# Performance work log

Hardware: AMD Instinct MI355X
Metric: run time of the kernel (lower is better)

## Reference

```python
import jax, jax.numpy as jnp
import numpy as np

N, H, DH = 8, 12, 64          # batch, heads, head dim (embedding_dim=768)
LV, LA = 1568, 512            # video / audio token counts
NCV, NCA = 392, 256           # candidates kept: LV*(1-0.75), LA*(1-0.5)
SCALE = DH ** -0.5            # avmatching_module.scale


def setup_inputs() -> dict:
    key = jax.random.key(0)
    ks = jax.random.split(key, 14)
    f32 = jnp.float32
    return {
        "pos_v_q": jax.random.normal(ks[0], (N, H, LV, DH), f32),
        "pos_v_k": jax.random.normal(ks[1], (N, H, LV, DH), f32),
        "pos_a_q": jax.random.normal(ks[2], (N, H, LA, DH), f32),
        "pos_a_k": jax.random.normal(ks[3], (N, H, LA, DH), f32),
        "pos_cross_att_av": jax.random.uniform(ks[4], (N, H, LA, LV), f32),
        "pos_cross_att_va": jax.random.uniform(ks[5], (N, H, LV, LA), f32),
        "n_attn_av": jax.random.uniform(ks[6], (N, LV), f32, 0.01, 1.0),
        "n_attn_va": jax.random.uniform(ks[7], (N, LA), f32, 0.01, 1.0),
        "spu_a_cls": jax.random.normal(ks[8], (N, H, DH), f32),
        "spu_v_cls": jax.random.normal(ks[9], (N, H, DH), f32),
        "u_v": jax.random.uniform(ks[10], (N, LV), f32),
        "u_a": jax.random.uniform(ks[11], (N, LA), f32),
        # att ids come from argsort of attention scores in the original -> permutations
        "att_av_ids": jnp.argsort(jax.random.uniform(ks[12], (N, LV)), axis=1),
        "att_va_ids": jnp.argsort(jax.random.uniform(ks[13], (N, LA)), axis=1),
    }


def _pipeline(pos_v_q, pos_v_k, pos_a_q, pos_a_k, pos_cross_att_av, pos_cross_att_va,
              n_attn_av, n_attn_va, spu_a_cls, spu_v_cls, u_v, u_a,
              att_av_ids, att_va_ids):
    idx_v = att_av_ids[:, :NCV]   # kept video token ids
    idx_a = att_va_ids[:, :NCA]   # kept audio token ids

    # --- gather kept tokens (torch.gather dim=2) and attention-weighted cls pooling ---
    d_v_k = jnp.take_along_axis(pos_v_k, idx_v[:, None, :, None], axis=2)   # [N,H,NCV,DH]
    v_tok = jnp.take_along_axis(pos_v_q, idx_v[:, None, :, None], axis=2)
    d_n_av = jnp.take_along_axis(n_attn_av, idx_v, axis=1)                  # [N,NCV]
    pos_v_cls = jnp.einsum('nhld,nl->nhd', v_tok, d_n_av) / jnp.sum(d_n_av, 1)[:, None, None]

    d_a_k = jnp.take_along_axis(pos_a_k, idx_a[:, None, :, None], axis=2)   # [N,H,NCA,DH]
    a_tok = jnp.take_along_axis(pos_a_q, idx_a[:, None, :, None], axis=2)
    d_n_va = jnp.take_along_axis(n_attn_va, idx_a, axis=1)                  # [N,NCA]
    pos_a_cls = jnp.einsum('nhld,nl->nhd', a_tok, d_n_va) / jnp.sum(d_n_va, 1)[:, None, None]

    # --- video keep probability: spurious (buffer audio query) vs positive attention ---
    v_spu = jnp.einsum('nhld,nhd->nhl', d_v_k, spu_a_cls) * SCALE           # [N,H,NCV]
    v_pos = jnp.take_along_axis(pos_cross_att_av, idx_v[:, None, None, :], axis=3)  # [N,H,LA,NCV]
    v_pos = jnp.take_along_axis(v_pos, idx_a[:, None, :, None], axis=2)     # [N,H,NCA,NCV]
    v_pos = jnp.einsum('nhal,na->nhl', v_pos, d_n_va) / jnp.sum(d_n_va, 1)[:, None, None]
    v_att = jax.nn.softmax(jnp.stack([v_spu, v_pos], axis=-1), axis=-1).mean(axis=1)
    prob_v = v_att[..., 0]                                                  # [N,NCV]
    restore_v = jnp.argsort(att_av_ids, axis=1)
    prob_v_full = jnp.take_along_axis(
        jnp.concatenate([prob_v, jnp.zeros((prob_v.shape[0], LV - NCV), prob_v.dtype)], axis=1),
        restore_v, axis=1)                                                  # [N,LV]

    # --- audio keep probability: spurious (buffer video query) vs positive attention ---
    a_spu = jnp.einsum('nhld,nhd->nhl', d_a_k, spu_v_cls) * SCALE           # [N,H,NCA]
    a_pos = jnp.take_along_axis(pos_cross_att_va, idx_a[:, None, None, :], axis=3)  # [N,H,LV,NCA]
    a_pos = jnp.take_along_axis(a_pos, idx_v[:, None, :, None], axis=2)     # [N,H,NCV,NCA]
    a_pos = jnp.einsum('nhvl,nv->nhl', a_pos, d_n_av) / jnp.sum(d_n_av, 1)[:, None, None]
    a_att = jax.nn.softmax(jnp.stack([a_spu, a_pos], axis=-1), axis=-1).mean(axis=1)
    prob_a = a_att[..., 0]                                                  # [N,NCA]
    restore_a = jnp.argsort(att_va_ids, axis=1)
    prob_a_full = jnp.take_along_axis(
        jnp.concatenate([prob_a, jnp.zeros((prob_a.shape[0], LA - NCA), prob_a.dtype)], axis=1),
        restore_a, axis=1)                                                  # [N,LA]

    # --- bernoulli pruning, deterministic via external uniforms (u < p == bernoulli(p)) ---
    prune_n_av = jnp.where(u_v < prob_v_full, 0.0, n_attn_av)
    prune_n_va = jnp.where(u_a < prob_a_full, 0.0, n_attn_va)

    n = prob_v_full.shape[0]
    return jnp.concatenate([prob_v_full, prob_a_full,
                            pos_v_cls.reshape(n, -1), pos_a_cls.reshape(n, -1),
                            prune_n_av, prune_n_va], axis=1)


def reference(pos_v_q, pos_v_k, pos_a_q, pos_a_k, pos_cross_att_av, pos_cross_att_va,
              n_attn_av, n_attn_va, spu_a_cls, spu_v_cls, u_v, u_a,
              att_av_ids, att_va_ids):
    return _pipeline(pos_v_q, pos_v_k, pos_a_q, pos_a_k, pos_cross_att_av,
                     pos_cross_att_va, n_attn_av, n_attn_va, spu_a_cls, spu_v_cls,
                     u_v, u_a, att_av_ids, att_va_ids)
```

## Files before the change

### kernel.cpp

```cpp
#include <hip/hip_runtime.h>

#define NN 8
#define HH 12
#define DH 64
#define LV 1568
#define LA 512
#define NCV 392
#define NCA 256
#define SCALE 0.125f

#define OUT_STRIDE (LV + LA + 2 * HH * DH + LV + LA)
#define OFF_PROB_V 0
#define OFF_PROB_A (LV)
#define OFF_VCLS   (LV + LA)
#define OFF_ACLS   (LV + LA + HH * DH)
#define OFF_PR_AV  (LV + LA + 2 * HH * DH)
#define OFF_PR_VA  (LV + LA + 2 * HH * DH + LV)

#define WS_RV      0
#define WS_RA      (NN * HH * LV)
#define WS_INV_SAV (WS_RA + NN * HH * LA)
#define WS_INV_SVA (WS_INV_SAV + NN)

#define CHA 8
#define CHV 8

__global__ __launch_bounds__(256) void init_kernel(
        const float* __restrict__ n_av,
        const float* __restrict__ n_va,
        const int* __restrict__ av_ids,
        const int* __restrict__ va_ids,
        float* __restrict__ ws) {
    int t = threadIdx.x;
    int idx = blockIdx.x * 256 + t;
    const int total4 = (NN * HH * LV + NN * HH * LA) / 4;
    if (idx < total4) ((float4*)ws)[idx] = make_float4(0.f, 0.f, 0.f, 0.f);

    if (blockIdx.x < NN) {
        int n = blockIdx.x;
        float vs = 0.f, as = 0.f;
        for (int l = t; l < NCV; l += 256) vs += n_av[n * LV + av_ids[n * LV + l]];
        if (t < NCA) as = n_va[n * LA + va_ids[n * LA + t]];
        for (int m = 32; m; m >>= 1) { vs += __shfl_xor(vs, m); as += __shfl_xor(as, m); }
        __shared__ float sv[4], sa[4];
        int wave = t >> 6;
        if ((t & 63) == 0) { sv[wave] = vs; sa[wave] = as; }
        __syncthreads();
        if (t == 0) {
            float S0 = sv[0] + sv[1] + sv[2] + sv[3];
            float S1 = sa[0] + sa[1] + sa[2] + sa[3];
            ws[WS_INV_SAV + n] = 1.f / S0;
            ws[WS_INV_SVA + n] = 1.f / S1;
        }
    }
}

__global__ __launch_bounds__(256) void rowsum_kernel(
        const float* __restrict__ av,
        const float* __restrict__ va,
        const int* __restrict__ av_ids,
        const int* __restrict__ va_ids,
        const float* __restrict__ n_av,
        const float* __restrict__ n_va,
        float* __restrict__ ws) {
    int b = blockIdx.x;
    int t = threadIdx.x;
    if (b < NN * HH * CHA) {
        int chunk = b % CHA;
        int nh    = b / CHA;
        int n     = nh / HH;
        const int rows = NCA / CHA;
        float4 acc0 = {0.f, 0.f, 0.f, 0.f};
        float4 acc1 = {0.f, 0.f, 0.f, 0.f};
        const int c0 = t;
        const int c1 = t + 256;
        const bool has1 = (c1 < LV / 4);
        for (int r = 0; r < rows; ++r) {
            int a = chunk * rows + r;
            int ridx = va_ids[n * LA + a];
            float w  = n_va[n * LA + ridx];
            const float4* row = (const float4*)(av + ((size_t)nh * LA + ridx) * LV);
            float4 x0 = row[c0];
            acc0.x += x0.x * w; acc0.y += x0.y * w; acc0.z += x0.z * w; acc0.w += x0.w * w;
            if (has1) {
                float4 x1 = row[c1];
                acc1.x += x1.x * w; acc1.y += x1.y * w; acc1.z += x1.z * w; acc1.w += x1.w * w;
            }
        }
        float* out = ws + WS_RV + (size_t)nh * LV;
        atomicAdd(&out[c0 * 4 + 0], acc0.x);
        atomicAdd(&out[c0 * 4 + 1], acc0.y);
        atomicAdd(&out[c0 * 4 + 2], acc0.z);
        atomicAdd(&out[c0 * 4 + 3], acc0.w);
        if (has1) {
            atomicAdd(&out[c1 * 4 + 0], acc1.x);
            atomicAdd(&out[c1 * 4 + 1], acc1.y);
            atomicAdd(&out[c1 * 4 + 2], acc1.z);
            atomicAdd(&out[c1 * 4 + 3], acc1.w);
        }
    } else {
        int b2    = b - NN * HH * CHA;
        int chunk = b2 % CHV;
        int nh    = b2 / CHV;
        int n     = nh / HH;
        const int rows = NCV / CHV;
        float2 acc = {0.f, 0.f};
        const int c = t;
        for (int r = 0; r < rows; ++r) {
            int v = chunk * rows + r;
            int ridx = av_ids[n * LV + v];
            float w  = n_av[n * LV + ridx];
            const float2* row = (const float2*)(va + ((size_t)nh * LV + ridx) * LA);
            float2 x = row[c];
            acc.x += x.x * w; acc.y += x.y * w;
        }
        float* out = ws + WS_RA + (size_t)nh * LA;
        atomicAdd(&out[c * 2 + 0], acc.x);
        atomicAdd(&out[c * 2 + 1], acc.y);
    }
}

__global__ __launch_bounds__(256) void cls_kernel(
        const float* __restrict__ pvq,
        const float* __restrict__ paq,
        const int* __restrict__ av_ids,
        const int* __restrict__ va_ids,
        const float* __restrict__ n_av,
        const float* __restrict__ n_va,
        float* __restrict__ out) {
    int b = blockIdx.x;
    int t = threadIdx.x;
    int wave = t >> 6, lane = t & 63;
    __shared__ float red[4][DH];
    __shared__ float wred[4];
    if (b < NN * HH) {
        int n = b / HH, h = b % HH;
        float acc = 0.f, wsum = 0.f;
        for (int l = wave; l < NCV; l += 4) {
            int ridx = av_ids[n * LV + l];
            float w  = n_av[n * LV + ridx];
            acc  += pvq[((size_t)b * LV + ridx) * DH + lane] * w;
            wsum += w;
        }
        red[wave][lane] = acc;
        if (lane == 0) wred[wave] = wsum;
        __syncthreads();
        if (wave == 0) {
            float s = red[0][lane] + red[1][lane] + red[2][lane] + red[3][lane];
            float W = wred[0] + wred[1] + wred[2] + wred[3];
            out[(size_t)n * OUT_STRIDE + OFF_VCLS + h * DH + lane] = s / W;
        }
    } else {
        int b2 = b - NN * HH;
        int n = b2 / HH, h = b2 % HH;
        float acc = 0.f, wsum = 0.f;
        for (int l = wave; l < NCA; l += 4) {
            int ridx = va_ids[n * LA + l];
            float w  = n_va[n * LA + ridx];
            acc  += paq[((size_t)b2 * LA + ridx) * DH + lane] * w;
            wsum += w;
        }
        red[wave][lane] = acc;
        if (lane == 0) wred[wave] = wsum;
        __syncthreads();
        if (wave == 0) {
            float s = red[0][lane] + red[1][lane] + red[2][lane] + red[3][lane];
            float W = wred[0] + wred[1] + wred[2] + wred[3];
            out[(size_t)n * OUT_STRIDE + OFF_ACLS + h * DH + lane] = s / W;
        }
    }
}

__global__ __launch_bounds__(256) void prob_kernel(
        const float* __restrict__ pvk,
        const float* __restrict__ pak,
        const float* __restrict__ spu_a,
        const float* __restrict__ spu_v,
        const int* __restrict__ av_ids,
        const int* __restrict__ va_ids,
        const float* __restrict__ n_av,
        const float* __restrict__ n_va,
        const float* __restrict__ u_v,
        const float* __restrict__ u_a,
        const float* __restrict__ ws,
        float* __restrict__ out) {
    int W = blockIdx.x * 4 + (threadIdx.x >> 6);
    int lane = threadIdx.x & 63;
    const int TV = NN * LV;
    if (W < TV) {
        int n = W / LV, l = W % LV;
        int col = av_ids[n * LV + l];
        float p = 0.f;
        if (l < NCV) {
            float invS = ws[WS_INV_SVA + n];
            float psum = 0.f;
            #pragma unroll
            for (int h = 0; h < HH; ++h) {
                int nh = n * HH + h;
                float prod = pvk[((size_t)nh * LV + col) * DH + lane] * spu_a[nh * DH + lane];
                for (int m = 32; m; m >>= 1) prod += __shfl_xor(prod, m);
                float spu = prod * SCALE;
                float pos = ws[WS_RV + (size_t)nh * LV + col] * invS;
                psum += 1.f / (1.f + __expf(pos - spu));
            }
            p = psum * (1.f / HH);
        }
        if (lane == 0) {
            out[(size_t)n * OUT_STRIDE + OFF_PROB_V + col] = p;
            float uv = u_v[n * LV + col];
            out[(size_t)n * OUT_STRIDE + OFF_PR_AV + col] =
                (uv < p) ? 0.f : n_av[n * LV + col];
        }
    } else {
        int W2 = W - TV;
        int n = W2 / LA, l = W2 % LA;
        int col = va_ids[n * LA + l];
        float p = 0.f;
        if (l < NCA) {
            float invS = ws[WS_INV_SAV + n];
            float psum = 0.f;
            #pragma unroll
            for (int h = 0; h < HH; ++h) {
                int nh = n * HH + h;
                float prod = pak[((size_t)nh * LA + col) * DH + lane] * spu_v[nh * DH + lane];
                for (int m = 32; m; m >>= 1) prod += __shfl_xor(prod, m);
                float spu = prod * SCALE;
                float pos = ws[WS_RA + (size_t)nh * LA + col] * invS;
                psum += 1.f / (1.f + __expf(pos - spu));
            }
            p = psum * (1.f / HH);
        }
        if (lane == 0) {
            out[(size_t)n * OUT_STRIDE + OFF_PROB_A + col] = p;
            float ua = u_a[n * LA + col];
            out[(size_t)n * OUT_STRIDE + OFF_PR_VA + col] =
                (ua < p) ? 0.f : n_va[n * LA + col];
        }
    }
}

extern "C" void kernel_launch(void* const* d_in, const int* in_sizes, int n_in,
                              void* d_out, int out_size, void* d_ws, size_t ws_size,
                              hipStream_t stream) {
    const float* pvq   = (const float*)d_in[0];
    const float* pvk   = (const float*)d_in[1];
    const float* paq   = (const float*)d_in[2];
    const float* pak   = (const float*)d_in[3];
    const float* av    = (const float*)d_in[4];
    const float* va    = (const float*)d_in[5];
    const float* n_av  = (const float*)d_in[6];
    const float* n_va  = (const float*)d_in[7];
    const float* spu_a = (const float*)d_in[8];
    const float* spu_v = (const float*)d_in[9];
    const float* u_v   = (const float*)d_in[10];
    const float* u_a   = (const float*)d_in[11];
    const int* av_ids  = (const int*)d_in[12];
    const int* va_ids  = (const int*)d_in[13];
    float* out = (float*)d_out;
    float* ws  = (float*)d_ws;

    init_kernel<<<256, 256, 0, stream>>>(n_av, n_va, av_ids, va_ids, ws);
    rowsum_kernel<<<NN * HH * (CHA + CHV), 256, 0, stream>>>(av, va, av_ids, va_ids,
                                                             n_av, n_va, ws);
    cls_kernel<<<2 * NN * HH, 256, 0, stream>>>(pvq, paq, av_ids, va_ids,
                                                n_av, n_va, out);
    prob_kernel<<<NN * (LV + LA) / 4, 256, 0, stream>>>(pvk, pak, spu_a, spu_v,
                                                        av_ids, va_ids, n_av, n_va,
                                                        u_v, u_a, ws, out);
}
```

Baseline: 648.1 us.

## Fuse init, rowsum and cls stages; replace atomics with per-chunk partial sums

Merges the init, rowsum and cls kernels into a single stage1 kernel that dispatches on block index. The zero-init pass and the atomicAdds go away: each chunk writes its partial rowsum to its own workspace slice, and prob_kernel adds up the CHA/CHV partials. Kept-row indices and weights are staged in shared memory, and the row loop is unrolled. prob_kernel now launches heavy waves only for kept tokens, while the pruned-token tail is handled by cheap per-thread blocks. In exchange there is more workspace traffic and more loads in the prob stage.

```diff
diff --git a/kernel.cpp b/kernel.cpp
--- a/kernel.cpp
+++ b/kernel.cpp
@@ -17,69 +17,119 @@
 #define OFF_PR_AV  (LV + LA + 2 * HH * DH)
 #define OFF_PR_VA  (LV + LA + 2 * HH * DH + LV)
 
-#define WS_RV      0
-#define WS_RA      (NN * HH * LV)
-#define WS_INV_SAV (WS_RA + NN * HH * LA)
-#define WS_INV_SVA (WS_INV_SAV + NN)
-
 #define CHA 8
 #define CHV 8
 
-__global__ __launch_bounds__(256) void init_kernel(
-        const float* __restrict__ n_av,
-        const float* __restrict__ n_va,
-        const int* __restrict__ av_ids,
-        const int* __restrict__ va_ids,
-        float* __restrict__ ws) {
-    int t = threadIdx.x;
-    int idx = blockIdx.x * 256 + t;
-    const int total4 = (NN * HH * LV + NN * HH * LA) / 4;
-    if (idx < total4) ((float4*)ws)[idx] = make_float4(0.f, 0.f, 0.f, 0.f);
-
-    if (blockIdx.x < NN) {
-        int n = blockIdx.x;
-        float vs = 0.f, as = 0.f;
-        for (int l = t; l < NCV; l += 256) vs += n_av[n * LV + av_ids[n * LV + l]];
-        if (t < NCA) as = n_va[n * LA + va_ids[n * LA + t]];
-        for (int m = 32; m; m >>= 1) { vs += __shfl_xor(vs, m); as += __shfl_xor(as, m); }
-        __shared__ float sv[4], sa[4];
-        int wave = t >> 6;
-        if ((t & 63) == 0) { sv[wave] = vs; sa[wave] = as; }
-        __syncthreads();
-        if (t == 0) {
-            float S0 = sv[0] + sv[1] + sv[2] + sv[3];
-            float S1 = sa[0] + sa[1] + sa[2] + sa[3];
-            ws[WS_INV_SAV + n] = 1.f / S0;
-            ws[WS_INV_SVA + n] = 1.f / S1;
-        }
-    }
-}
-
-__global__ __launch_bounds__(256) void rowsum_kernel(
+#define WS_RV      0
+#define WS_RA      (CHA * NN * HH * LV)
+#define WS_INV_SAV (WS_RA + CHV * NN * HH * LA)
+#define WS_INV_SVA (WS_INV_SAV + NN)
+
+#define B_INV   NN
+#define B_CLS   (2 * NN * HH)
+#define B_RAV   (NN * HH * CHA)
+#define B_RVA   (NN * HH * CHV)
+#define GRID_S1 (B_INV + B_CLS + B_RAV + B_RVA)
+
+__global__ __launch_bounds__(256) void stage1_kernel(
+        const float* __restrict__ pvq,
+        const float* __restrict__ paq,
         const float* __restrict__ av,
         const float* __restrict__ va,
         const int* __restrict__ av_ids,
         const int* __restrict__ va_ids,
         const float* __restrict__ n_av,
         const float* __restrict__ n_va,
-        float* __restrict__ ws) {
+        float* __restrict__ ws,
+        float* __restrict__ out) {
     int b = blockIdx.x;
     int t = threadIdx.x;
-    if (b < NN * HH * CHA) {
+    __shared__ float red[4][DH];
+    __shared__ float wred[4];
+    __shared__ int   sIdx[64];
+    __shared__ float sW[64];
+
+    if (b < B_INV) {
+        int n = b;
+        float vs = 0.f, as = 0.f;
+        for (int l = t; l < NCV; l += 256) vs += n_av[n * LV + av_ids[n * LV + l]];
+        if (t < NCA) as = n_va[n * LA + va_ids[n * LA + t]];
+        for (int m = 32; m; m >>= 1) { vs += __shfl_xor(vs, m); as += __shfl_xor(as, m); }
+        int wave = t >> 6;
+        if ((t & 63) == 0) { red[wave][0] = vs; wred[wave] = as; }
+        __syncthreads();
+        if (t == 0) {
+            float S0 = red[0][0] + red[1][0] + red[2][0] + red[3][0];
+            float S1 = wred[0] + wred[1] + wred[2] + wred[3];
+            ws[WS_INV_SAV + n] = 1.f / S0;
+            ws[WS_INV_SVA + n] = 1.f / S1;
+        }
+        return;
+    }
+    b -= B_INV;
+
+    if (b < B_CLS) {
+        int wave = t >> 6, lane = t & 63;
+        if (b < NN * HH) {
+            int n = b / HH, h = b % HH;
+            float acc = 0.f, wsum = 0.f;
+            for (int l = wave; l < NCV; l += 4) {
+                int ridx = av_ids[n * LV + l];
+                float w  = n_av[n * LV + ridx];
+                acc  += pvq[((size_t)b * LV + ridx) * DH + lane] * w;
+                wsum += w;
+            }
+            red[wave][lane] = acc;
+            if (lane == 0) wred[wave] = wsum;
+            __syncthreads();
+            if (wave == 0) {
+                float s = red[0][lane] + red[1][lane] + red[2][lane] + red[3][lane];
+                float W = wred[0] + wred[1] + wred[2] + wred[3];
+                out[(size_t)n * OUT_STRIDE + OFF_VCLS + h * DH + lane] = s / W;
+            }
+        } else {
+            int b2 = b - NN * HH;
+            int n = b2 / HH, h = b2 % HH;
+            float acc = 0.f, wsum = 0.f;
+            for (int l = wave; l < NCA; l += 4) {
+                int ridx = va_ids[n * LA + l];
+                float w  = n_va[n * LA + ridx];
+                acc  += paq[((size_t)b2 * LA + ridx) * DH + lane] * w;
+                wsum += w;
+            }
+            red[wave][lane] = acc;
+            if (lane == 0) wred[wave] = wsum;
+            __syncthreads();
+            if (wave == 0) {
+                float s = red[0][lane] + red[1][lane] + red[2][lane] + red[3][lane];
+                float W = wred[0] + wred[1] + wred[2] + wred[3];
+                out[(size_t)n * OUT_STRIDE + OFF_ACLS + h * DH + lane] = s / W;
+            }
+        }
+        return;
+    }
+    b -= B_CLS;
+
+    if (b < B_RAV) {
         int chunk = b % CHA;
         int nh    = b / CHA;
         int n     = nh / HH;
         const int rows = NCA / CHA;
+        if (t < rows) {
+            int ridx = va_ids[n * LA + chunk * rows + t];
+            sIdx[t] = ridx;
+            sW[t]   = n_va[n * LA + ridx];
+        }
+        __syncthreads();
         float4 acc0 = {0.f, 0.f, 0.f, 0.f};
         float4 acc1 = {0.f, 0.f, 0.f, 0.f};
         const int c0 = t;
         const int c1 = t + 256;
         const bool has1 = (c1 < LV / 4);
+        #pragma unroll 4
         for (int r = 0; r < rows; ++r) {
-            int a = chunk * rows + r;
-            int ridx = va_ids[n * LA + a];
-            float w  = n_va[n * LA + ridx];
-            const float4* row = (const float4*)(av + ((size_t)nh * LA + ridx) * LV);
+            float w = sW[r];
+            const float4* row = (const float4*)(av + ((size_t)nh * LA + sIdx[r]) * LV);
             float4 x0 = row[c0];
             acc0.x += x0.x * w; acc0.y += x0.y * w; acc0.z += x0.z * w; acc0.w += x0.w * w;
             if (has1) {
@@ -87,89 +137,42 @@
                 acc1.x += x1.x * w; acc1.y += x1.y * w; acc1.z += x1.z * w; acc1.w += x1.w * w;
             }
         }
-        float* out = ws + WS_RV + (size_t)nh * LV;
-        atomicAdd(&out[c0 * 4 + 0], acc0.x);
-        atomicAdd(&out[c0 * 4 + 1], acc0.y);
-        atomicAdd(&out[c0 * 4 + 2], acc0.z);
-        atomicAdd(&out[c0 * 4 + 3], acc0.w);
-        if (has1) {
-            atomicAdd(&out[c1 * 4 + 0], acc1.x);
-            atomicAdd(&out[c1 * 4 + 1], acc1.y);
-            atomicAdd(&out[c1 * 4 + 2], acc1.z);
-            atomicAdd(&out[c1 * 4 + 3], acc1.w);
-        }
-    } else {
-        int b2    = b - NN * HH * CHA;
-        int chunk = b2 % CHV;
-        int nh    = b2 / CHV;
+        float4* outp = (float4*)(ws + WS_RV + ((size_t)chunk * NN * HH + nh) * LV);
+        outp[c0] = acc0;
+        if (has1) outp[c1] = acc1;
+        return;
+    }
+    b -= B_RAV;
+
+    {
+        int chunk = b % CHV;
+        int nh    = b / CHV;
         int n     = nh / HH;
         const int rows = NCV / CHV;
+        if (t < rows) {
+            int ridx = av_ids[n * LV + chunk * rows + t];
+            sIdx[t] = ridx;
+            sW[t]   = n_av[n * LV + ridx];
+        }
+        __syncthreads();
         float2 acc = {0.f, 0.f};
-        const int c = t;
+        #pragma unroll 4
         for (int r = 0; r < rows; ++r) {
-            int v = chunk * rows + r;
-            int ridx = av_ids[n * LV + v];
-            float w  = n_av[n * LV + ridx];
-            const float2* row = (const float2*)(va + ((size_t)nh * LV + ridx) * LA);
-            float2 x = row[c];
+            float w = sW[r];
+            const float2* row = (const float2*)(va + ((size_t)nh * LV + sIdx[r]) * LA);
+            float2 x = row[t];
             acc.x += x.x * w; acc.y += x.y * w;
         }
-        float* out = ws + WS_RA + (size_t)nh * LA;
-        atomicAdd(&out[c * 2 + 0], acc.x);
-        atomicAdd(&out[c * 2 + 1], acc.y);
+        ((float2*)(ws + WS_RA + ((size_t)chunk * NN * HH + nh) * LA))[t] = acc;
     }
 }
 
-__global__ __launch_bounds__(256) void cls_kernel(
-        const float* __restrict__ pvq,
-        const float* __restrict__ paq,
-        const int* __restrict__ av_ids,
-        const int* __restrict__ va_ids,
-        const float* __restrict__ n_av,
-        const float* __restrict__ n_va,
-        float* __restrict__ out) {
-    int b = blockIdx.x;
-    int t = threadIdx.x;
-    int wave = t >> 6, lane = t & 63;
-    __shared__ float red[4][DH];
-    __shared__ float wred[4];
-    if (b < NN * HH) {
-        int n = b / HH, h = b % HH;
-        float acc = 0.f, wsum = 0.f;
-        for (int l = wave; l < NCV; l += 4) {
-            int ridx = av_ids[n * LV + l];
-            float w  = n_av[n * LV + ridx];
-            acc  += pvq[((size_t)b * LV + ridx) * DH + lane] * w;
-            wsum += w;
-        }
-        red[wave][lane] = acc;
-        if (lane == 0) wred[wave] = wsum;
-        __syncthreads();
-        if (wave == 0) {
-            float s = red[0][lane] + red[1][lane] + red[2][lane] + red[3][lane];
-            float W = wred[0] + wred[1] + wred[2] + wred[3];
-            out[(size_t)n * OUT_STRIDE + OFF_VCLS + h * DH + lane] = s / W;
-        }
-    } else {
-        int b2 = b - NN * HH;
-        int n = b2 / HH, h = b2 % HH;
-        float acc = 0.f, wsum = 0.f;
-        for (int l = wave; l < NCA; l += 4) {
-            int ridx = va_ids[n * LA + l];
-            float w  = n_va[n * LA + ridx];
-            acc  += paq[((size_t)b2 * LA + ridx) * DH + lane] * w;
-            wsum += w;
-        }
-        red[wave][lane] = acc;
-        if (lane == 0) wred[wave] = wsum;
-        __syncthreads();
-        if (wave == 0) {
-            float s = red[0][lane] + red[1][lane] + red[2][lane] + red[3][lane];
-            float W = wred[0] + wred[1] + wred[2] + wred[3];
-            out[(size_t)n * OUT_STRIDE + OFF_ACLS + h * DH + lane] = s / W;
-        }
-    }
-}
+#define MAIN_W  (NN * NCV + NN * NCA)
+#define MAIN_B  (MAIN_W / 4)
+#define TAILV   (NN * (LV - NCV))
+#define TAILA   (NN * (LA - NCA))
+#define TAIL_B  ((TAILV + TAILA + 255) / 256)
+#define GRID_PB (MAIN_B + TAIL_B)
 
 __global__ __launch_bounds__(256) void prob_kernel(
         const float* __restrict__ pvk,
@@ -184,14 +187,12 @@
         const float* __restrict__ u_a,
         const float* __restrict__ ws,
         float* __restrict__ out) {
-    int W = blockIdx.x * 4 + (threadIdx.x >> 6);
-    int lane = threadIdx.x & 63;
-    const int TV = NN * LV;
-    if (W < TV) {
-        int n = W / LV, l = W % LV;
-        int col = av_ids[n * LV + l];
-        float p = 0.f;
-        if (l < NCV) {
+    if (blockIdx.x < MAIN_B) {
+        int W = blockIdx.x * 4 + (threadIdx.x >> 6);
+        int lane = threadIdx.x & 63;
+        if (W < NN * NCV) {
+            int n = W / NCV, l = W % NCV;
+            int col = av_ids[n * LV + l];
             float invS = ws[WS_INV_SVA + n];
             float psum = 0.f;
             #pragma unroll
@@ -199,24 +200,23 @@
                 int nh = n * HH + h;
                 float prod = pvk[((size_t)nh * LV + col) * DH + lane] * spu_a[nh * DH + lane];
                 for (int m = 32; m; m >>= 1) prod += __shfl_xor(prod, m);
-                float spu = prod * SCALE;
-                float pos = ws[WS_RV + (size_t)nh * LV + col] * invS;
-                psum += 1.f / (1.f + __expf(pos - spu));
-            }
-            p = psum * (1.f / HH);
-        }
-        if (lane == 0) {
-            out[(size_t)n * OUT_STRIDE + OFF_PROB_V + col] = p;
-            float uv = u_v[n * LV + col];
-            out[(size_t)n * OUT_STRIDE + OFF_PR_AV + col] =
-                (uv < p) ? 0.f : n_av[n * LV + col];
-        }
-    } else {
-        int W2 = W - TV;
-        int n = W2 / LA, l = W2 % LA;
-        int col = va_ids[n * LA + l];
-        float p = 0.f;
-        if (l < NCA) {
+                float pos = 0.f;
+                #pragma unroll
+                for (int p = 0; p < CHA; ++p)
+                    pos += ws[WS_RV + ((size_t)p * NN * HH + nh) * LV + col];
+                psum += 1.f / (1.f + __expf(pos * invS - prod * SCALE));
+            }
+            float pm = psum * (1.f / HH);
+            if (lane == 0) {
+                out[(size_t)n * OUT_STRIDE + OFF_PROB_V + col] = pm;
+                float uv = u_v[n * LV + col];
+                out[(size_t)n * OUT_STRIDE + OFF_PR_AV + col] =
+                    (uv < pm) ? 0.f : n_av[n * LV + col];
+            }
+        } else {
+            int W2 = W - NN * NCV;
+            int n = W2 / NCA, l = W2 % NCA;
+            int col = va_ids[n * LA + l];
             float invS = ws[WS_INV_SAV + n];
             float psum = 0.f;
             #pragma unroll
@@ -224,17 +224,33 @@
                 int nh = n * HH + h;
                 float prod = pak[((size_t)nh * LA + col) * DH + lane] * spu_v[nh * DH + lane];
                 for (int m = 32; m; m >>= 1) prod += __shfl_xor(prod, m);
-                float spu = prod * SCALE;
-                float pos = ws[WS_RA + (size_t)nh * LA + col] * invS;
-                psum += 1.f / (1.f + __expf(pos - spu));
-            }
-            p = psum * (1.f / HH);
-        }
-        if (lane == 0) {
-            out[(size_t)n * OUT_STRIDE + OFF_PROB_A + col] = p;
-            float ua = u_a[n * LA + col];
-            out[(size_t)n * OUT_STRIDE + OFF_PR_VA + col] =
-                (ua < p) ? 0.f : n_va[n * LA + col];
+                float pos = 0.f;
+                #pragma unroll
+                for (int p = 0; p < CHV; ++p)
+                    pos += ws[WS_RA + ((size_t)p * NN * HH + nh) * LA + col];
+                psum += 1.f / (1.f + __expf(pos * invS - prod * SCALE));
+            }
+            float pm = psum * (1.f / HH);
+            if (lane == 0) {
+                out[(size_t)n * OUT_STRIDE + OFF_PROB_A + col] = pm;
+                float ua = u_a[n * LA + col];
+                out[(size_t)n * OUT_STRIDE + OFF_PR_VA + col] =
+                    (ua < pm) ? 0.f : n_va[n * LA + col];
+            }
+        }
+    } else {
+        int tid = (blockIdx.x - MAIN_B) * 256 + threadIdx.x;
+        if (tid < TAILV) {
+            int n = tid / (LV - NCV), l = NCV + tid % (LV - NCV);
+            int col = av_ids[n * LV + l];
+            out[(size_t)n * OUT_STRIDE + OFF_PROB_V + col] = 0.f;
+            out[(size_t)n * OUT_STRIDE + OFF_PR_AV + col] = n_av[n * LV + col];
+        } else if (tid < TAILV + TAILA) {
+            int i = tid - TAILV;
+            int n = i / (LA - NCA), l = NCA + i % (LA - NCA);
+            int col = va_ids[n * LA + l];
+            out[(size_t)n * OUT_STRIDE + OFF_PROB_A + col] = 0.f;
+            out[(size_t)n * OUT_STRIDE + OFF_PR_VA + col] = n_va[n * LA + col];
         }
     }
 }
@@ -259,12 +275,9 @@
     float* out = (float*)d_out;
     float* ws  = (float*)d_ws;
 
-    init_kernel<<<256, 256, 0, stream>>>(n_av, n_va, av_ids, va_ids, ws);
-    rowsum_kernel<<<NN * HH * (CHA + CHV), 256, 0, stream>>>(av, va, av_ids, va_ids,
-                                                             n_av, n_va, ws);
-    cls_kernel<<<2 * NN * HH, 256, 0, stream>>>(pvq, paq, av_ids, va_ids,
-                                                n_av, n_va, out);
-    prob_kernel<<<NN * (LV + LA) / 4, 256, 0, stream>>>(pvk, pak, spu_a, spu_v,
-                                                        av_ids, va_ids, n_av, n_va,
-                                                        u_v, u_a, ws, out);
+    stage1_kernel<<<GRID_S1, 256, 0, stream>>>(pvq, paq, av, va, av_ids, va_ids,
+                                               n_av, n_va, ws, out);
+    prob_kernel<<<GRID_PB, 256, 0, stream>>>(pvk, pak, spu_a, spu_v,
+                                             av_ids, va_ids, n_av, n_va,
+                                             u_v, u_a, ws, out);
 }
```

After: 628.4 us. 3.0% less time.
